# Optimization experiments

Measured on AMD Instinct MI355X. Metric: run time of the kernel, lower is better.

The kernel has to match this reference:

```python
import jax, jax.numpy as jnp
import numpy as np

B, S, D, H = 1, 2048, 4096, 32
HD = D // H  # 128


def _rope_params(seq_len, head_dim, base=10000.0):
    inv_freq = 1.0 / (base ** (np.arange(0, head_dim, 2, dtype=np.float64) / head_dim))
    ang = np.outer(np.arange(seq_len, dtype=np.float64), inv_freq)      # [S, HD/2]
    ang = np.concatenate([ang, ang], axis=-1)                            # [S, HD]
    return jnp.asarray(np.cos(ang), jnp.float32), jnp.asarray(np.sin(ang), jnp.float32)


def _apply_rope(x, cos, sin):
    # x: [B, H, S, HD]; cos/sin: [S, HD]
    half = x.shape[-1] // 2
    x1, x2 = x[..., :half], x[..., half:]
    rotated = jnp.concatenate([-x2, x1], axis=-1)
    return x * cos[None, None] + rotated * sin[None, None]


def setup_inputs() -> dict:
    key = jax.random.key(0)
    ks = jax.random.split(key, 6)
    w_scale = 1.0 / np.sqrt(D)
    X = jax.random.normal(ks[0], (B, S, D), jnp.float32)
    Wq = jax.random.normal(ks[1], (D, D), jnp.float32) * w_scale
    Wk = jax.random.normal(ks[2], (D, D), jnp.float32) * w_scale
    Wv = jax.random.normal(ks[3], (D, D), jnp.float32) * w_scale
    Wo = jax.random.normal(ks[4], (D, D), jnp.float32) * w_scale
    bo = jax.random.normal(ks[5], (D,), jnp.float32) * 0.01
    cos, sin = _rope_params(S, HD)
    return {"X": X, "Wq": Wq, "Wk": Wk, "Wv": Wv, "Wo": Wo, "bo": bo, "cos": cos, "sin": sin}


def reference(X, Wq, Wk, Wv, Wo, bo, cos, sin):
    b, s, d = X.shape
    # nn.Linear: y = x @ W.T
    def split_heads(y):
        return y.reshape(b, s, H, HD).transpose(0, 2, 1, 3)  # [B,H,S,HD]
    q = split_heads(X @ Wq.T)
    k = split_heads(X @ Wk.T)
    v = split_heads(X @ Wv.T)
    q = _apply_rope(q, cos, sin)
    k = _apply_rope(k, cos, sin)
    scores = jnp.einsum('bhqd,bhkd->bhqk', q, k) / np.sqrt(HD).astype(np.float32)
    causal = jnp.tril(jnp.ones((s, s), bool))
    scores = jnp.where(causal[None, None], scores, -jnp.inf)
    attn = jax.nn.softmax(scores, axis=-1)
    out = jnp.einsum('bhqk,bhkd->bhqd', attn, v)  # [B,H,S,HD]
    out = out.transpose(0, 2, 1, 3).reshape(b, s, d)
    return out @ Wo.T + bo
```

## Files before the change

### kernel.cpp

```cpp
#include <hip/hip_runtime.h>

typedef unsigned short u16;
typedef __attribute__((ext_vector_type(8))) short s16x8;
typedef __attribute__((ext_vector_type(4))) float f32x4;

__device__ __forceinline__ u16 f2bf(float f) {
  unsigned u = __float_as_uint(f);
  u += 0x7fffu + ((u >> 16) & 1u);
  return (u16)(u >> 16);
}
__device__ __forceinline__ float bf2f(u16 h) {
  return __uint_as_float(((unsigned)h) << 16);
}
__device__ __forceinline__ unsigned pk2(float lo, float hi) {
  return ((__float_as_uint(hi) + 0x8000u) & 0xffff0000u) |
         ((__float_as_uint(lo) + 0x8000u) >> 16);
}

typedef __attribute__((address_space(1))) const void gvoid_t;
typedef __attribute__((address_space(3))) void lvoid_t;
__device__ __forceinline__ void gload_lds16(const void* g, void* l) {
  __builtin_amdgcn_global_load_lds((gvoid_t*)g, (lvoid_t*)l, 16, 0, 0);
}

__global__ void cvt_f32_bf16(const float* __restrict__ in, u16* __restrict__ out, int n) {
  int i = (blockIdx.x * 256 + threadIdx.x) * 4;
  if (i >= n) return;
  float4 v = *(const float4*)(in + i);
  ushort4 o;
  o.x = f2bf(v.x); o.y = f2bf(v.y); o.z = f2bf(v.z); o.w = f2bf(v.w);
  *(ushort4*)(out + i) = o;
}

__global__ void cvt4(const float* __restrict__ X,
                     const float* __restrict__ Wq, const float* __restrict__ Wk,
                     const float* __restrict__ Wv,
                     u16* __restrict__ Xb, u16* __restrict__ WB3) {
  long i = ((long)blockIdx.x * 256 + threadIdx.x) * 4;
  const float* src; u16* dst; long off;
  if (i < (1L << 23)) { src = X; dst = Xb; off = i; }
  else {
    long k = i - (1L << 23);
    int w = (int)(k >> 24);
    off = k & ((1L << 24) - 1);
    src = (w == 0) ? Wq : (w == 1) ? Wk : Wv;
    dst = WB3 + ((size_t)w << 24);
  }
  float4 v = *(const float4*)(src + off);
  ushort4 o;
  o.x = f2bf(v.x); o.y = f2bf(v.y); o.z = f2bf(v.z); o.w = f2bf(v.w);
  *(ushort4*)(dst + off) = o;
}

template<typename OutT, bool BIAS>
__global__ __launch_bounds__(256) void gemm_bt3(
    const u16* __restrict__ A, const u16* __restrict__ Bm,
    OutT* __restrict__ C, const float* __restrict__ bias,
    int M, int N, int K)
{
  __shared__ u16 As[3][128 * 32];
  __shared__ u16 Bs[3][128 * 32];

  const int t = threadIdx.x;
  const int lane = t & 63, wid = t >> 6;
  const int wm = wid >> 1, wn = wid & 1;
  const int lr = lane & 15, lk = lane >> 4;

  const int wg = blockIdx.x;
  const int xcd = wg & 7, j = wg >> 3;
  const int m0 = (j & 15) * 128;
  const int n0 = ((xcd << 2) | (j >> 4)) * 128;

  const int nt = K >> 5;

  f32x4 acc[4][4] = {};

#define STAGE3(KT)                                                             \
  {                                                                            \
    const int bu_ = (KT) % 3;                                                  \
    const int k0_ = (KT) << 5;                                                 \
    _Pragma("unroll")                                                          \
    for (int it = 0; it < 2; ++it) {                                           \
      int id = it * 256 + t;                                                   \
      int r = id >> 2, c0 = id & 3;                                            \
      int cs = (c0 ^ ((r >> 1) & 3)) << 3;                                     \
      gload_lds16(A + (size_t)(m0 + r) * K + k0_ + cs, &As[bu_][id * 8]);      \
      gload_lds16(Bm + (size_t)(n0 + r) * K + k0_ + cs, &Bs[bu_][id * 8]);     \
    }                                                                          \
  }

  STAGE3(0);
  STAGE3(1);
  asm volatile("s_waitcnt vmcnt(4)" ::: "memory");
  __builtin_amdgcn_s_barrier();

  for (int kt = 0; kt < nt; ++kt) {
    const int bu = kt % 3;
    if (kt + 2 < nt) STAGE3(kt + 2);

    s16x8 af[4], bf[4];
#pragma unroll
    for (int i = 0; i < 4; ++i) {
      int ra = wm * 64 + i * 16 + lr;
      af[i] = *(const s16x8*)&As[bu][ra * 32 + ((lk ^ ((ra >> 1) & 3)) << 3)];
      int rb = wn * 64 + i * 16 + lr;
      bf[i] = *(const s16x8*)&Bs[bu][rb * 32 + ((lk ^ ((rb >> 1) & 3)) << 3)];
    }
    __builtin_amdgcn_s_setprio(1);
#pragma unroll
    for (int i = 0; i < 4; ++i)
#pragma unroll
      for (int jn = 0; jn < 4; ++jn)
        acc[i][jn] = __builtin_amdgcn_mfma_f32_16x16x32_bf16(af[i], bf[jn], acc[i][jn], 0, 0, 0);
    __builtin_amdgcn_s_setprio(0);

    asm volatile("s_waitcnt lgkmcnt(0)" ::: "memory");
    if (kt + 2 < nt)       { asm volatile("s_waitcnt vmcnt(4)" ::: "memory"); }
    else if (kt + 2 == nt) { asm volatile("s_waitcnt vmcnt(0)" ::: "memory"); }
    if (kt + 1 < nt) __builtin_amdgcn_s_barrier();
  }
#undef STAGE3

#pragma unroll
  for (int i = 0; i < 4; ++i) {
    int row_b = m0 + wm * 64 + i * 16 + lk * 4;
#pragma unroll
    for (int jn = 0; jn < 4; ++jn) {
      int col = n0 + wn * 64 + jn * 16 + lr;
      float bv = BIAS ? bias[col] : 0.f;
#pragma unroll
      for (int r = 0; r < 4; ++r) {
        float v = acc[i][jn][r] + bv;
        size_t off = (size_t)(row_b + r) * N + col;
        if constexpr (sizeof(OutT) == 2) ((u16*)C)[off] = f2bf(v);
        else                             ((float*)C)[off] = v;
      }
    }
  }
}

__global__ __launch_bounds__(256) void gemm_qkv(
    const u16* __restrict__ A, const u16* __restrict__ Bstk,
    u16* __restrict__ Qb, u16* __restrict__ Kb, u16* __restrict__ Vb,
    int M, int K)
{
  __shared__ u16 As[3][128 * 32];
  __shared__ u16 Bs[3][128 * 32];

  const int t = threadIdx.x;
  const int lane = t & 63, wid = t >> 6;
  const int wm = wid >> 1, wn = wid & 1;
  const int lr = lane & 15, lk = lane >> 4;

  const int wg = blockIdx.x;
  const int xcd = wg & 7, j = wg >> 3;
  const int m0 = (j & 15) * 128;
  const int n0 = (xcd * 12 + (j >> 4)) * 128;

  const int nt = K >> 5;

  f32x4 acc[4][4] = {};

#define STAGEQ(KT)                                                             \
  {                                                                            \
    const int bu_ = (KT) % 3;                                                  \
    const int k0_ = (KT) << 5;                                                 \
    _Pragma("unroll")                                                          \
    for (int it = 0; it < 2; ++it) {                                           \
      int id = it * 256 + t;                                                   \
      int r = id >> 2, c0 = id & 3;                                            \
      int cs = (c0 ^ ((r >> 1) & 3)) << 3;                                     \
      gload_lds16(A + (size_t)(m0 + r) * K + k0_ + cs, &As[bu_][id * 8]);      \
      gload_lds16(Bstk + (size_t)(n0 + r) * K + k0_ + cs, &Bs[bu_][id * 8]);   \
    }                                                                          \
  }

  STAGEQ(0);
  STAGEQ(1);
  asm volatile("s_waitcnt vmcnt(4)" ::: "memory");
  __builtin_amdgcn_s_barrier();

  for (int kt = 0; kt < nt; ++kt) {
    const int bu = kt % 3;
    if (kt + 2 < nt) STAGEQ(kt + 2);

    s16x8 af[4], bf[4];
#pragma unroll
    for (int i = 0; i < 4; ++i) {
      int ra = wm * 64 + i * 16 + lr;
      af[i] = *(const s16x8*)&As[bu][ra * 32 + ((lk ^ ((ra >> 1) & 3)) << 3)];
      int rb = wn * 64 + i * 16 + lr;
      bf[i] = *(const s16x8*)&Bs[bu][rb * 32 + ((lk ^ ((rb >> 1) & 3)) << 3)];
    }
    __builtin_amdgcn_s_setprio(1);
#pragma unroll
    for (int i = 0; i < 4; ++i)
#pragma unroll
      for (int jn = 0; jn < 4; ++jn)
        acc[i][jn] = __builtin_amdgcn_mfma_f32_16x16x32_bf16(af[i], bf[jn], acc[i][jn], 0, 0, 0);
    __builtin_amdgcn_s_setprio(0);

    asm volatile("s_waitcnt lgkmcnt(0)" ::: "memory");
    if (kt + 2 < nt)       { asm volatile("s_waitcnt vmcnt(4)" ::: "memory"); }
    else if (kt + 2 == nt) { asm volatile("s_waitcnt vmcnt(0)" ::: "memory"); }
    if (kt + 1 < nt) __builtin_amdgcn_s_barrier();
  }
#undef STAGEQ

  u16* Cp; int nb;
  if (n0 < 4096)      { Cp = Qb; nb = n0; }
  else if (n0 < 8192) { Cp = Kb; nb = n0 - 4096; }
  else                { Cp = Vb; nb = n0 - 8192; }

#pragma unroll
  for (int i = 0; i < 4; ++i) {
    int row_b = m0 + wm * 64 + i * 16 + lk * 4;
#pragma unroll
    for (int jn = 0; jn < 4; ++jn) {
      int col = nb + wn * 64 + jn * 16 + lr;
#pragma unroll
      for (int r = 0; r < 4; ++r)
        Cp[(size_t)(row_b + r) * 4096 + col] = f2bf(acc[i][jn][r]);
    }
  }
}

__global__ void rope_qk(u16* __restrict__ Q, u16* __restrict__ Kt,
                        const float* __restrict__ cosp, const float* __restrict__ sinp) {
  int i = blockIdx.x * 256 + threadIdx.x;
  int d = i & 63;
  int h = (i >> 6) & 31;
  int s = i >> 11;
  float c = cosp[s * 128 + d], sn = sinp[s * 128 + d];
  size_t base = (size_t)s * 4096 + h * 128 + d;
  float q1 = bf2f(Q[base]), q2 = bf2f(Q[base + 64]);
  Q[base]      = f2bf(q1 * c - q2 * sn);
  Q[base + 64] = f2bf(q2 * c + q1 * sn);
  float k1 = bf2f(Kt[base]), k2 = bf2f(Kt[base + 64]);
  Kt[base]      = f2bf(k1 * c - k2 * sn);
  Kt[base + 64] = f2bf(k2 * c + k1 * sn);
}

__global__ __launch_bounds__(256) void flash_attn(
    const u16* __restrict__ Q, const u16* __restrict__ Kg, const u16* __restrict__ Vg,
    u16* __restrict__ Ctx)
{
  const int D = 4096;
  __shared__ u16 Ks[2][64 * 128];
  __shared__ u16 Vt[128 * 64];

  const int t = threadIdx.x, lane = t & 63, wid = t >> 6;
  const int lr = lane & 15, lk = lane >> 4;

  const int wg = blockIdx.x;
  const int xcd = wg & 7, j = wg >> 3;
  const int bx = 31 - (j >> 2);
  const int h = xcd * 4 + (j & 3);
  const int q0 = bx * 64;
  const int qw0 = q0 + wid * 16;

  s16x8 qf[4];
#pragma unroll
  for (int kc = 0; kc < 4; ++kc)
    qf[kc] = *(const s16x8*)(Q + (size_t)(qw0 + lr) * D + h * 128 + kc * 32 + lk * 8);

  f32x4 o[8] = {};
  float m_s = -1e30f, l_s = 0.f;

  const int ntiles = bx + 1;
  const float scale2 = 0.12751779f;

  const int ch = t & 15, kv4 = (t >> 4) * 4;

  {
#pragma unroll
    for (int it = 0; it < 4; ++it) {
      int id = it * 256 + t;
      int kv = id >> 4, c0 = id & 15;
      gload_lds16(Kg + (size_t)kv * D + h * 128 + ((c0 ^ (kv & 7)) << 3), &Ks[0][id * 8]);
    }
    const u16* src = Vg + (size_t)kv4 * D + h * 128 + ch * 8;
    s16x8 v0 = *(const s16x8*)src;
    s16x8 v1 = *(const s16x8*)(src + D);
    s16x8 v2 = *(const s16x8*)(src + 2 * D);
    s16x8 v3 = *(const s16x8*)(src + 3 * D);
#pragma unroll
    for (int jj = 0; jj < 8; ++jj) {
      int d = ch * 8 + jj;
      int sw = ((ch ^ jj) & 7) << 3;
      *(unsigned*)&Vt[d * 64 + ((kv4)     ^ sw)] = (unsigned)(u16)v0[jj] | ((unsigned)(u16)v1[jj] << 16);
      *(unsigned*)&Vt[d * 64 + ((kv4 + 2) ^ sw)] = (unsigned)(u16)v2[jj] | ((unsigned)(u16)v3[jj] << 16);
    }
  }

  for (int kt = 0; kt < ntiles; ++kt) {
    const int b = kt & 1;
    const int kv0 = kt * 64;
    __syncthreads();

    s16x8 v0, v1, v2, v3;
    const bool pf = (kt + 1 < ntiles);
    if (pf) {
      const u16* src = Vg + (size_t)(kv0 + 64 + kv4) * D + h * 128 + ch * 8;
      v0 = *(const s16x8*)src;
      v1 = *(const s16x8*)(src + D);
      v2 = *(const s16x8*)(src + 2 * D);
      v3 = *(const s16x8*)(src + 3 * D);
#pragma unroll
      for (int it = 0; it < 4; ++it) {
        int id = it * 256 + t;
        int kv = id >> 4, c0 = id & 15;
        gload_lds16(Kg + (size_t)(kv0 + 64 + kv) * D + h * 128 + ((c0 ^ (kv & 7)) << 3),
                    &Ks[b ^ 1][id * 8]);
      }
    }

    if (kv0 <= qw0 + 15) {
      const bool masked = (kv0 + 63 > qw0);

      f32x4 st[4] = {};
      __builtin_amdgcn_s_setprio(1);
#pragma unroll
      for (int nt = 0; nt < 4; ++nt) {
        int kv = nt * 16 + lr;
        int sw = kv & 7;
#pragma unroll
        for (int kc = 0; kc < 4; ++kc) {
          s16x8 kf = *(const s16x8*)&Ks[b][kv * 128 + (((4 * kc + lk) ^ sw) << 3)];
          st[nt] = __builtin_amdgcn_mfma_f32_16x16x32_bf16(kf, qf[kc], st[nt], 0, 0, 0);
        }
      }
      __builtin_amdgcn_s_setprio(0);

      float pm = -1e30f;
#pragma unroll
      for (int nt = 0; nt < 4; ++nt)
#pragma unroll
        for (int r = 0; r < 4; ++r) {
          float sv = st[nt][r] * scale2;
          if (masked && (kv0 + nt * 16 + lk * 4 + r > qw0 + lr)) sv = -1e30f;
          st[nt][r] = sv;
          pm = fmaxf(pm, sv);
        }
      pm = fmaxf(pm, __shfl_xor(pm, 16));
      pm = fmaxf(pm, __shfl_xor(pm, 32));

      if (__any(pm > m_s + 8.f)) {
        float mn = fmaxf(m_s, pm);
        float al = __builtin_amdgcn_exp2f(m_s - mn);
        m_s = mn; l_s *= al;
        float aq0 = __shfl(al, (lane & 48) | (lk * 4 + 0));
        float aq1 = __shfl(al, (lane & 48) | (lk * 4 + 1));
        float aq2 = __shfl(al, (lane & 48) | (lk * 4 + 2));
        float aq3 = __shfl(al, (lane & 48) | (lk * 4 + 3));
#pragma unroll
        for (int nb = 0; nb < 8; ++nb) {
          o[nb][0] *= aq0; o[nb][1] *= aq1; o[nb][2] *= aq2; o[nb][3] *= aq3;
        }
      }

      float ps = 0.f;
#pragma unroll
      for (int nt = 0; nt < 4; ++nt)
#pragma unroll
        for (int r = 0; r < 4; ++r) {
          float pv = __builtin_amdgcn_exp2f(st[nt][r] - m_s);
          st[nt][r] = pv;
          ps += pv;
        }
      ps += __shfl_xor(ps, 16);
      ps += __shfl_xor(ps, 32);
      l_s += ps;

      unsigned pkv[4][2];
#pragma unroll
      for (int nt = 0; nt < 4; ++nt) {
        pkv[nt][0] = pk2(st[nt][0], st[nt][1]);
        pkv[nt][1] = pk2(st[nt][2], st[nt][3]);
      }

      const int srcA = lr | (((lk & 1) * 2) << 4);
      const int srcB = srcA + 16;
      const bool sel = (lk >> 1) != 0;
      s16x8 pa[2];
#pragma unroll
      for (int ks = 0; ks < 2; ++ks) {
        int a0 = __shfl((int)pkv[ks * 2][0], srcA);
        int b0 = __shfl((int)pkv[ks * 2 + 1][0], srcA);
        int a1 = __shfl((int)pkv[ks * 2][1], srcA);
        int b1 = __shfl((int)pkv[ks * 2 + 1][1], srcA);
        int a2 = __shfl((int)pkv[ks * 2][0], srcB);
        int b2 = __shfl((int)pkv[ks * 2 + 1][0], srcB);
        int a3 = __shfl((int)pkv[ks * 2][1], srcB);
        int b3 = __shfl((int)pkv[ks * 2 + 1][1], srcB);
        int4 w = { sel ? b0 : a0, sel ? b1 : a1, sel ? b2 : a2, sel ? b3 : a3 };
        pa[ks] = *(s16x8*)&w;
      }

      __builtin_amdgcn_s_setprio(1);
#pragma unroll
      for (int ks = 0; ks < 2; ++ks) {
#pragma unroll
        for (int nb = 0; nb < 8; ++nb) {
          int d = nb * 16 + lr;
          int g = (((d >> 3) ^ d) & 7) << 3;
          s16x8 vf = *(const s16x8*)&Vt[d * 64 + ((ks * 32 + lk * 8) ^ g)];
          o[nb] = __builtin_amdgcn_mfma_f32_16x16x32_bf16(pa[ks], vf, o[nb], 0, 0, 0);
        }
      }
      __builtin_amdgcn_s_setprio(0);
    }

    if (pf) {
      __builtin_amdgcn_s_barrier();
#pragma unroll
      for (int jj = 0; jj < 8; ++jj) {
        int d = ch * 8 + jj;
        int sw = ((ch ^ jj) & 7) << 3;
        *(unsigned*)&Vt[d * 64 + ((kv4)     ^ sw)] = (unsigned)(u16)v0[jj] | ((unsigned)(u16)v1[jj] << 16);
        *(unsigned*)&Vt[d * 64 + ((kv4 + 2) ^ sw)] = (unsigned)(u16)v2[jj] | ((unsigned)(u16)v3[jj] << 16);
      }
    }
  }

  float linv = 1.f / l_s;
  float i0 = __shfl(linv, (lane & 48) | (lk * 4 + 0));
  float i1 = __shfl(linv, (lane & 48) | (lk * 4 + 1));
  float i2 = __shfl(linv, (lane & 48) | (lk * 4 + 2));
  float i3 = __shfl(linv, (lane & 48) | (lk * 4 + 3));
#pragma unroll
  for (int nb = 0; nb < 8; ++nb) {
    int d = h * 128 + nb * 16 + lr;
    Ctx[(size_t)(qw0 + lk * 4 + 0) * D + d] = f2bf(o[nb][0] * i0);
    Ctx[(size_t)(qw0 + lk * 4 + 1) * D + d] = f2bf(o[nb][1] * i1);
    Ctx[(size_t)(qw0 + lk * 4 + 2) * D + d] = f2bf(o[nb][2] * i2);
    Ctx[(size_t)(qw0 + lk * 4 + 3) * D + d] = f2bf(o[nb][3] * i3);
  }
}

extern "C" void kernel_launch(void* const* d_in, const int* in_sizes, int n_in,
                              void* d_out, int out_size, void* d_ws, size_t ws_size,
                              hipStream_t stream) {
  const int S = 2048, D = 4096, H = 32;
  const size_t SD = (size_t)S * D, DD = (size_t)D * D;

  const float* X  = (const float*)d_in[0];
  const float* Wq = (const float*)d_in[1];
  const float* Wk = (const float*)d_in[2];
  const float* Wv = (const float*)d_in[3];
  const float* Wo = (const float*)d_in[4];
  const float* bo = (const float*)d_in[5];
  const float* cs = (const float*)d_in[6];
  const float* sn = (const float*)d_in[7];

  dim3 blk(256);
  dim3 g3(512);
  dim3 b3(256);

  const size_t need_fused = (3 * DD + 4 * SD) * sizeof(u16);

  if (ws_size >= need_fused) {
    u16* WB3 = (u16*)d_ws;
    u16* Xb  = WB3 + 3 * DD;
    u16* Qb  = Xb + SD;
    u16* Kb  = Qb + SD;
    u16* Vb  = Kb + SD;

    cvt4<<<(int)((SD + 3 * DD) / 1024), blk, 0, stream>>>(X, Wq, Wk, Wv, Xb, WB3);

    gemm_qkv<<<dim3(1536), b3, 0, stream>>>(Xb, WB3, Qb, Kb, Vb, S, D);

    rope_qk<<<(S * H * 64) / 256, blk, 0, stream>>>(Qb, Kb, cs, sn);
    flash_attn<<<dim3(1024), dim3(256), 0, stream>>>(Qb, Kb, Vb, Xb );

    cvt_f32_bf16<<<(int)(DD / 1024), blk, 0, stream>>>(Wo, WB3, (int)DD);
    gemm_bt3<float, true><<<g3, b3, 0, stream>>>(Xb, WB3, (float*)d_out, bo, S, D, D);
  } else {
    u16* WB = (u16*)d_ws;
    u16* Xb = WB + DD;
    u16* Qb = Xb + SD;
    u16* Kb = Qb + SD;
    u16* Vb = Kb + SD;

    cvt_f32_bf16<<<(int)(SD / 1024), blk, 0, stream>>>(X, Xb, (int)SD);
    cvt_f32_bf16<<<(int)(DD / 1024), blk, 0, stream>>>(Wq, WB, (int)DD);
    gemm_bt3<u16, false><<<g3, b3, 0, stream>>>(Xb, WB, Qb, nullptr, S, D, D);
    cvt_f32_bf16<<<(int)(DD / 1024), blk, 0, stream>>>(Wk, WB, (int)DD);
    gemm_bt3<u16, false><<<g3, b3, 0, stream>>>(Xb, WB, Kb, nullptr, S, D, D);
    cvt_f32_bf16<<<(int)(DD / 1024), blk, 0, stream>>>(Wv, WB, (int)DD);
    gemm_bt3<u16, false><<<g3, b3, 0, stream>>>(Xb, WB, Vb, nullptr, S, D, D);

    rope_qk<<<(S * H * 64) / 256, blk, 0, stream>>>(Qb, Kb, cs, sn);
    flash_attn<<<dim3(1024), dim3(256), 0, stream>>>(Qb, Kb, Vb, Xb );

    cvt_f32_bf16<<<(int)(DD / 1024), blk, 0, stream>>>(Wo, WB, (int)DD);
    gemm_bt3<float, true><<<g3, b3, 0, stream>>>(Xb, WB, (float*)d_out, bo, S, D, D);
  }
}
```

Before: 483.5 us.

## Replace QKV GEMM with 256x256-tile, 8-wave kernel using quadrant-staged pipeline

```diff
diff --git a/kernel.cpp b/kernel.cpp
--- a/kernel.cpp
+++ b/kernel.cpp
@@ -135,6 +135,140 @@
         if constexpr (sizeof(OutT) == 2) ((u16*)C)[off] = f2bf(v);
         else                             ((float*)C)[off] = v;
       }
+    }
+  }
+}
+
+__global__ __launch_bounds__(512) void gemm_qkv8(
+    const u16* __restrict__ A, const u16* __restrict__ Bstk,
+    u16* __restrict__ Qb, u16* __restrict__ Kb, u16* __restrict__ Vb)
+{
+  const int K = 4096;
+  __shared__ u16 As[2][2][128 * 64];
+  __shared__ u16 Bs[2][2][128 * 64];
+
+  const int t = threadIdx.x;
+  const int lane = t & 63, wid = t >> 6;
+  const int wm = wid >> 2, wn = wid & 3;
+  const int lr = lane & 15, lk = lane >> 4;
+
+  const int wg = blockIdx.x;
+  const int xcd = wg & 7, j = wg >> 3;
+  const int m0 = (j & 7) * 256;
+  const int n0 = (xcd * 6 + (j >> 3)) * 256;
+
+  const int sr = t >> 3, sc = t & 7;
+
+  f32x4 acc[8][4] = {};
+  s16x8 af[4][2], bf[2][2];
+
+#define STAGE_K(kind, T)                                                       \
+  {                                                                            \
+    const int bu_ = (T) & 1, k0_ = (T) << 6;                                   \
+    u16* slab_ = (kind) == 0 ? &As[bu_][0][0] : (kind) == 1 ? &Bs[bu_][1][0]   \
+               : (kind) == 2 ? &Bs[bu_][0][0] : &As[bu_][1][0];                \
+    const u16* src_ = ((kind) == 0 || (kind) == 3) ? A : Bstk;                 \
+    const int rb_ = (kind) == 0 ? m0 : (kind) == 1 ? n0 + 128                  \
+                  : (kind) == 2 ? n0 : m0 + 128;                               \
+    _Pragma("unroll")                                                          \
+    for (int it = 0; it < 2; ++it) {                                           \
+      int r_ = it * 64 + sr;                                                   \
+      gload_lds16(src_ + (size_t)(rb_ + r_) * K + k0_ + ((sc ^ (r_ & 7)) << 3),\
+                  slab_ + (it * 512 + t) * 8);                                 \
+    }                                                                          \
+  }
+
+#define RD_A(mh, bu)                                                           \
+  _Pragma("unroll")                                                            \
+  for (int f = 0; f < 4; ++f) {                                                \
+    int rA = f * 32 + wm * 16 + lr;                                            \
+    _Pragma("unroll")                                                          \
+    for (int ks = 0; ks < 2; ++ks)                                             \
+      af[f][ks] = *(const s16x8*)&As[bu][mh][rA * 64 +                         \
+                    (((ks * 4 + lk) ^ (rA & 7)) << 3)];                        \
+  }
+#define RD_B(nh, bu)                                                           \
+  _Pragma("unroll")                                                            \
+  for (int e = 0; e < 2; ++e) {                                                \
+    int rB = e * 64 + wn * 16 + lr;                                            \
+    _Pragma("unroll")                                                          \
+    for (int ks = 0; ks < 2; ++ks)                                             \
+      bf[e][ks] = *(const s16x8*)&Bs[bu][nh][rB * 64 +                         \
+                    (((ks * 4 + lk) ^ (rB & 7)) << 3)];                        \
+  }
+#define BAR_LGKM()                                                             \
+  __builtin_amdgcn_s_barrier();                                                \
+  asm volatile("s_waitcnt lgkmcnt(0)" ::: "memory");                           \
+  __builtin_amdgcn_sched_barrier(0);
+#define MM(mh, nh)                                                             \
+  __builtin_amdgcn_s_setprio(1);                                               \
+  _Pragma("unroll")                                                            \
+  for (int f = 0; f < 4; ++f)                                                  \
+    _Pragma("unroll")                                                          \
+    for (int e = 0; e < 2; ++e)                                                \
+      _Pragma("unroll")                                                        \
+      for (int ks = 0; ks < 2; ++ks)                                           \
+        acc[(mh) * 4 + f][(nh) * 2 + e] =                                      \
+            __builtin_amdgcn_mfma_f32_16x16x32_bf16(                           \
+                af[f][ks], bf[e][ks], acc[(mh) * 4 + f][(nh) * 2 + e], 0, 0, 0);\
+  __builtin_amdgcn_s_setprio(0);
+
+  const int NT = K >> 6;
+
+  STAGE_K(0, 0); STAGE_K(1, 0); STAGE_K(2, 0); STAGE_K(3, 0);
+  STAGE_K(0, 1); STAGE_K(1, 1);
+  asm volatile("s_waitcnt vmcnt(4)" ::: "memory");
+  __builtin_amdgcn_s_barrier();
+
+  for (int tau = 0; tau < NT; ++tau) {
+    const int bu = tau & 1;
+
+    RD_A(0, bu); RD_B(0, bu);
+    if (tau + 1 < NT) STAGE_K(2, tau + 1);
+    BAR_LGKM();
+    MM(0, 0);
+    __builtin_amdgcn_s_barrier();
+
+    RD_B(1, bu);
+    if (tau + 1 < NT) STAGE_K(3, tau + 1);
+    BAR_LGKM();
+    MM(0, 1);
+    __builtin_amdgcn_s_barrier();
+
+    RD_A(1, bu);
+    if (tau + 2 < NT) STAGE_K(0, tau + 2);
+    BAR_LGKM();
+    MM(1, 1);
+    __builtin_amdgcn_s_barrier();
+
+    RD_B(0, bu);
+    if (tau + 2 < NT) STAGE_K(1, tau + 2);
+    BAR_LGKM();
+    MM(1, 0);
+    if (tau == NT - 2)     { asm volatile("s_waitcnt vmcnt(0)" ::: "memory"); }
+    else if (tau < NT - 1) { asm volatile("s_waitcnt vmcnt(4)" ::: "memory"); }
+    if (tau < NT - 1) __builtin_amdgcn_s_barrier();
+  }
+#undef STAGE_K
+#undef RD_A
+#undef RD_B
+#undef BAR_LGKM
+#undef MM
+
+  u16* Cp; int nb;
+  if (n0 < 4096)      { Cp = Qb; nb = n0; }
+  else if (n0 < 8192) { Cp = Kb; nb = n0 - 4096; }
+  else                { Cp = Vb; nb = n0 - 8192; }
+
+#pragma unroll
+  for (int F = 0; F < 8; ++F) {
+    int row_b = m0 + (F >> 2) * 128 + (F & 3) * 32 + wm * 16 + lk * 4;
+#pragma unroll
+    for (int E = 0; E < 4; ++E) {
+      int col = nb + (E >> 1) * 128 + (E & 1) * 64 + wn * 16 + lr;
+#pragma unroll
+      for (int r = 0; r < 4; ++r)
+        Cp[(size_t)(row_b + r) * 4096 + col] = f2bf(acc[F][E][r]);
     }
   }
 }
@@ -468,7 +602,7 @@
 
     cvt4<<<(int)((SD + 3 * DD) / 1024), blk, 0, stream>>>(X, Wq, Wk, Wv, Xb, WB3);
 
-    gemm_qkv<<<dim3(1536), b3, 0, stream>>>(Xb, WB3, Qb, Kb, Vb, S, D);
+    gemm_qkv8<<<dim3(384), dim3(512), 0, stream>>>(Xb, WB3, Qb, Kb, Vb);
 
     rope_qk<<<(S * H * 64) / 256, blk, 0, stream>>>(Qb, Kb, cs, sn);
     flash_attn<<<dim3(1024), dim3(256), 0, stream>>>(Qb, Kb, Vb, Xb );
```

Measured after the change: 569.0 us. +17.7%, slower.
